# Kernel optimization log

Measured on AMD Instinct MI355X. Metric: run time of the kernel, lower is better.

Reference implementation:

```python
import jax, jax.numpy as jnp
import numpy as np

B, CIN, HIN, WIN = 1, 26, 721, 1440
K, HOUT, KH, KW = 9, 360, 9, 9
COUT = 256
PSCALE = WIN // (WIN // 2)  # lon downsample stride = 2
WOUT = WIN // 2


def setup_inputs() -> dict:
    key = jax.random.key(0)
    k1, k2, k3 = jax.random.split(key, 3)
    x = jax.random.normal(k1, (B, CIN, HIN, WIN), dtype=jnp.float32)
    # precomputed basis*quadrature stencil psi[k, ho, dh, dw] (shift-invariant in lon,
    # stored only for wo=0, exactly as DISCO does). Normalized per (k, ho) ('mean' mode).
    psi = jax.random.normal(k2, (K, HOUT, KH, KW), dtype=jnp.float32)
    psi = psi / (jnp.mean(jnp.abs(psi), axis=(2, 3), keepdims=True) * (KH * KW) + 1e-6)
    weight = jax.random.normal(k3, (COUT, CIN, K), dtype=jnp.float32) * (1.0 / np.sqrt(CIN * K))
    # base input-lat row for each output lat (stencil top row), clipped to valid range
    hi_base = np.clip(np.round(np.arange(HOUT) * (HIN - 1) / HOUT).astype(np.int32) - KH // 2, 0, HIN - 1)
    return {"x": x, "psi": psi, "weight": weight, "hi_base": jnp.asarray(hi_base, dtype=jnp.int32)}


def _disco_conv(x, psi, weight, hi_base):
    x = x.astype(jnp.float32)  # fp32 autocast-off region, matches torch module
    acc = jnp.zeros((B, CIN, K, HOUT, WOUT), dtype=jnp.float32)
    for dh in range(KH):  # small structural loop over stencil rows
        rows = jnp.clip(hi_base + dh, 0, HIN - 1)  # [Hout]
        xr = x[:, :, rows, :]
        for dw in range(KW):  # small structural loop over stencil lon offsets
            shift = dw - KW // 2
            xs = jnp.roll(xr, -shift, axis=-1)[..., ::PSCALE]  # [B,C,Hout,Wout]
            acc = acc + psi[:, :, dh, dw][None, None, :, :, None] * xs[:, :, None, :, :]
    # contract learned weights over kernel basis and input channels
    out = jnp.einsum('bckhw,ock->bohw', acc, weight)  # [B,Cout,Hout,Wout]
    return out


def reference(x, psi, weight, hi_base):
    return _disco_conv(x, psi, weight, hi_base)
```

## Files before the change

### kernel.cpp

```cpp
#include <hip/hip_runtime.h>
#include <hip/hip_bf16.h>

#define CIN_   26
#define HIN_   721
#define WIN_   1440
#define K_     9
#define HOUT_  360
#define KH_    9
#define KW_    9
#define COUT_  256
#define WOUT_  720

#define WT     16
#define XFP    40
#define CCH    7
#define CK     (CIN_ * K_)
#define NKS2   9
#define ACCP2  296
#define NMT    (COUT_ / 16)
#define NXCD   8
#define HBAND  (HOUT_ / NXCD)

typedef short bf16x8 __attribute__((ext_vector_type(8)));
typedef float f32x4  __attribute__((ext_vector_type(4)));

__device__ unsigned short g_whi[NMT * NKS2 * 64 * 8];
__device__ unsigned short g_pfrag[HOUT_ * 3 * 64 * 8];

__device__ __forceinline__ unsigned short f2bf_rne(float f) {
    union { float f; unsigned u; } v; v.f = f;
    unsigned u = v.u;
    unsigned r = (u + 0x7FFFu + ((u >> 16) & 1u)) >> 16;
    return (unsigned short)r;
}
__device__ __forceinline__ unsigned pack_bf2(float a, float b) {
    const __hip_bfloat162 bv = __float22bfloat162_rn(make_float2(a, b));
    return *reinterpret_cast<const unsigned*>(&bv);
}
__device__ __forceinline__ void gload_lds16(const float* g, float* l) {
    __builtin_amdgcn_global_load_lds(
        (const __attribute__((address_space(1))) void*)g,
        (__attribute__((address_space(3))) void*)l,
        16, 0, 0);
}

__global__ void prep_weight_kernel(const float* __restrict__ weight) {
    const int bid  = blockIdx.x;
    const int mt   = bid / NKS2;
    const int ks   = bid % NKS2;
    const int lane = threadIdx.x;
    const int row  = mt * 16 + (lane & 15);
    const int k0   = ks * 32 + (lane >> 4) * 8;
    const int base = ((mt * NKS2 + ks) * 64 + lane) * 8;
    #pragma unroll
    for (int j = 0; j < 8; ++j) {
        const int kp = k0 + j;
        float w = 0.f;
        if (kp < 260) {
            const int c = kp / 10, m = kp % 10;
            if (m < 9) w = weight[row * CK + c * 9 + m];
        }
        g_whi[base + j] = f2bf_rne(w);
    }
}

__global__ void prep_psi_kernel(const float* __restrict__ psi) {
    const int h    = blockIdx.x;
    const int lane = threadIdx.x;
    const int m    = lane & 15;
    const int kg   = lane >> 4;
    #pragma unroll
    for (int ks = 0; ks < 3; ++ks) {
        const int base = ((h * 3 + ks) * 64 + lane) * 8;
        #pragma unroll
        for (int e = 0; e < 8; ++e) {
            const int s = ks * 32 + kg * 8 + e;
            float v = 0.f;
            if (m < 9) {
                if (s < 72)      v = psi[(m * HOUT_ + h) * 81 + (s >> 3) * 9 + (s & 7)];
                else if (s < 81) v = psi[(m * HOUT_ + h) * 81 + (s - 72) * 9 + 8];
            }
            g_pfrag[base + e] = f2bf_rne(v);
        }
    }
}

#define LDS_BARRIER()                                      \
    do {                                                   \
        asm volatile("s_waitcnt lgkmcnt(0)" ::: "memory"); \
        __builtin_amdgcn_s_barrier();                      \
    } while (0)
#define VM_WAIT(N) asm volatile("s_waitcnt vmcnt(" #N ")" ::: "memory")

__global__ __launch_bounds__(256, 4)
void disco_fused_kernel(const float* __restrict__ x,
                        const int*   __restrict__ hi_base,
                        float* __restrict__ out)
{
    __shared__ float xs_f[2][12 * 256];
    __shared__ __align__(16) unsigned short acc_s[WT][ACCP2];

    const int b    = blockIdx.x;
    const int xcd  = b & (NXCD - 1);
    const int jb   = b >> 3;
    const int h    = xcd * HBAND + jb / 45;
    const int tile = jb % 45;
    const int w0   = tile * WT;
    const int tid  = threadIdx.x;

    const int hib = hi_base[h];

    #pragma unroll
    for (int t = 0; t < 2; ++t) {
        const int e = tid + t * 256;
        if (e < 16 * 28) acc_s[e / 28][260 + e % 28] = 0;
    }

    const int lane = tid & 63;
    const int wid  = tid >> 6;
    const int n    = lane & 15;
    const int kg   = lane >> 4;

    bf16x8 afrag[3];
    #pragma unroll
    for (int ks = 0; ks < 3; ++ks)
        afrag[ks] = *(const bf16x8*)&g_pfrag[((h * 3 + ks) * 64 + lane) * 8];
    VM_WAIT(0);

    const int c0 = 2 * w0 - 4;

    #define ISSUE_DMA(RD, BUF, RMAX)                                             \
    do {                                                                         \
        const int cb = (RD) * CCH;                                               \
        _Pragma("unroll")                                                        \
        for (int it = 0; it < 3; ++it) {                                         \
            const int g64 = wid + 4 * it;                                        \
            const int ii  = g64 * 64 + lane;                                     \
            int row = ii / 10;                                                   \
            const int q = ii - row * 10;                                         \
            if (row > (RMAX)) row = (RMAX);                                      \
            const int dh = row % 9;                                              \
            const int c  = cb + row / 9;                                         \
            int r = hib + dh;                                                    \
            if (r > HIN_ - 1) r = HIN_ - 1;                                      \
            int gc = c0 + 4 * q;                                                 \
            if (gc < 0)          gc += WIN_;                                     \
            else if (gc >= WIN_) gc -= WIN_;                                     \
            gload_lds16(x + ((size_t)c * HIN_ + r) * WIN_ + gc,                  \
                        &xs_f[BUF][g64 * 256]);                                  \
        }                                                                        \
    } while (0)

    ISSUE_DMA(0, 0, 62);
    ISSUE_DMA(1, 1, 62);
    VM_WAIT(3);
    LDS_BARRIER();

    #pragma unroll
    for (int rd = 0; rd < 4; ++rd) {
        const int nc = (rd == 3) ? (CIN_ - 3 * CCH) : CCH;
        const float* xsf = &xs_f[rd & 1][0];

        for (int cc = wid; cc < nc; cc += 4) {
            const int c = rd * CCH + cc;
            const float* rbase = xsf + (cc * 9) * XFP + 2 * n;
            f32x4 C = {0.f, 0.f, 0.f, 0.f};
            #pragma unroll
            for (int ks = 0; ks < 3; ++ks) {
                union { bf16x8 v; unsigned d[4]; unsigned short u[8]; } bf;
                if (ks < 2 || kg == 0) {
                    const float* rp = rbase + (ks * 4 + kg) * XFP;
                    #pragma unroll
                    for (int t = 0; t < 4; ++t) {
                        const float2 v2 = *reinterpret_cast<const float2*>(rp + 2 * t);
                        bf.d[t] = pack_bf2(v2.x, v2.y);
                    }
                } else if (kg == 1) {
                    #pragma unroll
                    for (int e = 0; e < 8; ++e)
                        bf.u[e] = f2bf_rne(rbase[e * XFP + 8]);
                } else if (kg == 2) {
                    bf.d[0] = bf.d[1] = bf.d[2] = bf.d[3] = 0;
                    bf.u[0] = f2bf_rne(rbase[8 * XFP + 8]);
                } else {
                    bf.d[0] = bf.d[1] = bf.d[2] = bf.d[3] = 0;
                }
                C = __builtin_amdgcn_mfma_f32_16x16x32_bf16(afrag[ks], bf.v, C, 0, 0, 0);
            }
            if (kg < 2) {
                unsigned* ap = reinterpret_cast<unsigned*>(&acc_s[n][c * 10 + kg * 4]);
                ap[0] = pack_bf2(C[0], C[1]);
                ap[1] = pack_bf2(C[2], C[3]);
            } else if (kg == 2) {
                *reinterpret_cast<unsigned*>(&acc_s[n][c * 10 + 8]) = pack_bf2(C[0], 0.f);
            }
        }

        if (rd == 0) {
            LDS_BARRIER();
            ISSUE_DMA(2, 0, 62);
            VM_WAIT(3);
            LDS_BARRIER();
        } else if (rd == 1) {
            LDS_BARRIER();
            ISSUE_DMA(3, 1, 44);
            VM_WAIT(3);
            LDS_BARRIER();
        } else if (rd == 2) {
            LDS_BARRIER();
            VM_WAIT(0);
            LDS_BARRIER();
        }
    }
    #undef ISSUE_DMA
    LDS_BARRIER();

    f32x4 C0 = {0.f, 0.f, 0.f, 0.f};
    f32x4 C1 = C0, C2 = C0, C3 = C0;

    const unsigned short* wp = g_whi + ((size_t)(wid * 4) * NKS2 * 64 + lane) * 8;

    bf16x8 wc[4];
    #pragma unroll
    for (int i = 0; i < 4; ++i)
        wc[i] = *(const bf16x8*)(wp + (size_t)i * NKS2 * 512);

    #pragma unroll
    for (int ks = 0; ks < NKS2; ++ks) {
        bf16x8 wn[4];
        if (ks + 1 < NKS2) {
            #pragma unroll
            for (int i = 0; i < 4; ++i)
                wn[i] = *(const bf16x8*)(wp + ((size_t)i * NKS2 + (ks + 1)) * 512);
        }
        const bf16x8 bhi = *(const bf16x8*)&acc_s[n][ks * 32 + kg * 8];
        C0 = __builtin_amdgcn_mfma_f32_16x16x32_bf16(wc[0], bhi, C0, 0, 0, 0);
        C1 = __builtin_amdgcn_mfma_f32_16x16x32_bf16(wc[1], bhi, C1, 0, 0, 0);
        C2 = __builtin_amdgcn_mfma_f32_16x16x32_bf16(wc[2], bhi, C2, 0, 0, 0);
        C3 = __builtin_amdgcn_mfma_f32_16x16x32_bf16(wc[3], bhi, C3, 0, 0, 0);
        if (ks + 1 < NKS2) {
            #pragma unroll
            for (int i = 0; i < 4; ++i) wc[i] = wn[i];
        }
    }

    #pragma unroll
    for (int i = 0; i < 4; ++i) {
        const f32x4 acc = (i == 0) ? C0 : (i == 1) ? C1 : (i == 2) ? C2 : C3;
        const int m0 = (wid * 4 + i) * 16 + kg * 4;
        #pragma unroll
        for (int r = 0; r < 4; ++r) {
            out[(size_t)(m0 + r) * (HOUT_ * WOUT_) + h * WOUT_ + w0 + n] = acc[r];
        }
    }
}

extern "C" void kernel_launch(void* const* d_in, const int* in_sizes, int n_in,
                              void* d_out, int out_size, void* d_ws, size_t ws_size,
                              hipStream_t stream)
{
    const float* x       = (const float*)d_in[0];
    const float* psi     = (const float*)d_in[1];
    const float* weight  = (const float*)d_in[2];
    const int*   hi_base = (const int*)d_in[3];
    float* out = (float*)d_out;

    hipLaunchKernelGGL(prep_weight_kernel, dim3(NMT * NKS2), dim3(64), 0, stream, weight);
    hipLaunchKernelGGL(prep_psi_kernel,    dim3(HOUT_),      dim3(64), 0, stream, psi);

    dim3 grid(45 * HOUT_, 1, 1);
    dim3 block(256, 1, 1);
    hipLaunchKernelGGL(disco_fused_kernel, grid, block, 0, stream,
                       x, hi_base, out);
}
```

Before: 257.1 us.

## Process five lon tiles per block with double-buffered accumulator and overlapped phases

Each block now loops over five consecutive longitude tiles for one output latitude, which shrinks the grid from 16200 to 3240 blocks and amortises the psi fragment, weight pointer and setup cost. The accumulator in LDS is double-buffered so the channel-mixing MFMA and output store for the previous tile run between the stencil rounds of the current tile. The input DMA for the next tile is also prefetched during the current tile. In exchange LDS use grows, occupancy is lowered to 3 blocks, and the per-block serial chain gets longer.

```diff
diff --git a/kernel.cpp b/kernel.cpp
--- a/kernel.cpp
+++ b/kernel.cpp
@@ -19,7 +19,7 @@
 #define ACCP2  296
 #define NMT    (COUT_ / 16)
 #define NXCD   8
-#define HBAND  (HOUT_ / NXCD)
+#define TPB    5
 
 typedef short bf16x8 __attribute__((ext_vector_type(8)));
 typedef float f32x4  __attribute__((ext_vector_type(4)));
@@ -92,167 +92,185 @@
     } while (0)
 #define VM_WAIT(N) asm volatile("s_waitcnt vmcnt(" #N ")" ::: "memory")
 
-__global__ __launch_bounds__(256, 4)
+#define ISSUE(C0V, RD, BUF, RMAX)                                                \
+do {                                                                             \
+    const int cb = (RD) * CCH;                                                   \
+    _Pragma("unroll")                                                            \
+    for (int it = 0; it < 3; ++it) {                                             \
+        const int g64 = wid + 4 * it;                                            \
+        const int ii  = g64 * 64 + lane;                                         \
+        int row = ii / 10;                                                       \
+        const int q = ii - row * 10;                                             \
+        if (row > (RMAX)) row = (RMAX);                                          \
+        const int dh = row % 9;                                                  \
+        const int c  = cb + row / 9;                                             \
+        int r = hib + dh;                                                        \
+        if (r > HIN_ - 1) r = HIN_ - 1;                                          \
+        int gc = (C0V) + 4 * q;                                                  \
+        if (gc < 0)          gc += WIN_;                                         \
+        else if (gc >= WIN_) gc -= WIN_;                                         \
+        gload_lds16(x + ((size_t)c * HIN_ + r) * WIN_ + gc,                      \
+                    &xs_f[BUF][g64 * 256]);                                      \
+    }                                                                            \
+} while (0)
+
+#define P1_ROUND(RD, BUF, ACC)                                                   \
+do {                                                                             \
+    const int nc = ((RD) == 3) ? (CIN_ - 3 * CCH) : CCH;                         \
+    const float* xsf = &xs_f[BUF][0];                                            \
+    for (int cc = wid; cc < nc; cc += 4) {                                       \
+        const int c = (RD) * CCH + cc;                                           \
+        const float* rbase = xsf + (cc * 9) * XFP + 2 * n;                       \
+        f32x4 C = {0.f, 0.f, 0.f, 0.f};                                          \
+        _Pragma("unroll")                                                        \
+        for (int ks = 0; ks < 3; ++ks) {                                         \
+            union { bf16x8 v; unsigned d[4]; unsigned short u[8]; } bf;          \
+            if (ks < 2 || kg == 0) {                                             \
+                const float* rp = rbase + (ks * 4 + kg) * XFP;                   \
+                _Pragma("unroll")                                                \
+                for (int t2 = 0; t2 < 4; ++t2) {                                 \
+                    const float2 v2 = *reinterpret_cast<const float2*>(rp + 2 * t2); \
+                    bf.d[t2] = pack_bf2(v2.x, v2.y);                             \
+                }                                                                \
+            } else if (kg == 1) {                                                \
+                _Pragma("unroll")                                                \
+                for (int e = 0; e < 8; ++e)                                      \
+                    bf.u[e] = f2bf_rne(rbase[e * XFP + 8]);                      \
+            } else if (kg == 2) {                                                \
+                bf.d[0] = bf.d[1] = bf.d[2] = bf.d[3] = 0;                       \
+                bf.u[0] = f2bf_rne(rbase[8 * XFP + 8]);                          \
+            } else {                                                             \
+                bf.d[0] = bf.d[1] = bf.d[2] = bf.d[3] = 0;                       \
+            }                                                                    \
+            C = __builtin_amdgcn_mfma_f32_16x16x32_bf16(afrag[ks], bf.v, C, 0, 0, 0); \
+        }                                                                        \
+        if (kg < 2) {                                                            \
+            unsigned* ap = reinterpret_cast<unsigned*>(&ACC[n][c * 10 + kg * 4]);\
+            ap[0] = pack_bf2(C[0], C[1]);                                        \
+            ap[1] = pack_bf2(C[2], C[3]);                                        \
+        } else if (kg == 2) {                                                    \
+            *reinterpret_cast<unsigned*>(&ACC[n][c * 10 + 8]) = pack_bf2(C[0], 0.f); \
+        }                                                                        \
+    }                                                                            \
+} while (0)
+
+#define P2_STORE(TT)                                                             \
+do {                                                                             \
+    const unsigned short (*accp)[ACCP2] =                                        \
+        (const unsigned short (*)[ACCP2])acc_s[(TT) & 1];                        \
+    f32x4 C0 = {0.f, 0.f, 0.f, 0.f}, C1 = C0, C2 = C0, C3 = C0;                  \
+    bf16x8 wc[4];                                                                \
+    _Pragma("unroll")                                                            \
+    for (int i = 0; i < 4; ++i)                                                  \
+        wc[i] = *(const bf16x8*)(wp + (size_t)i * NKS2 * 512);                   \
+    _Pragma("unroll")                                                            \
+    for (int ks = 0; ks < NKS2; ++ks) {                                          \
+        bf16x8 wn[4];                                                            \
+        if (ks + 1 < NKS2) {                                                     \
+            _Pragma("unroll")                                                    \
+            for (int i = 0; i < 4; ++i)                                          \
+                wn[i] = *(const bf16x8*)(wp + ((size_t)i * NKS2 + (ks + 1)) * 512); \
+        }                                                                        \
+        const bf16x8 bhi = *(const bf16x8*)&accp[n][ks * 32 + kg * 8];           \
+        C0 = __builtin_amdgcn_mfma_f32_16x16x32_bf16(wc[0], bhi, C0, 0, 0, 0);   \
+        C1 = __builtin_amdgcn_mfma_f32_16x16x32_bf16(wc[1], bhi, C1, 0, 0, 0);   \
+        C2 = __builtin_amdgcn_mfma_f32_16x16x32_bf16(wc[2], bhi, C2, 0, 0, 0);   \
+        C3 = __builtin_amdgcn_mfma_f32_16x16x32_bf16(wc[3], bhi, C3, 0, 0, 0);   \
+        if (ks + 1 < NKS2) {                                                     \
+            _Pragma("unroll")                                                    \
+            for (int i = 0; i < 4; ++i) wc[i] = wn[i];                           \
+        }                                                                        \
+    }                                                                            \
+    const int w0s = (tile0 + (TT)) * WT;                                         \
+    _Pragma("unroll")                                                            \
+    for (int i = 0; i < 4; ++i) {                                                \
+        const f32x4 a2 = (i == 0) ? C0 : (i == 1) ? C1 : (i == 2) ? C2 : C3;     \
+        const int m0 = (wid * 4 + i) * 16 + kg * 4;                              \
+        _Pragma("unroll")                                                        \
+        for (int r = 0; r < 4; ++r)                                              \
+            out[(size_t)(m0 + r) * (HOUT_ * WOUT_) + h * WOUT_ + w0s + n] = a2[r]; \
+    }                                                                            \
+} while (0)
+
+__global__ __launch_bounds__(256, 3)
 void disco_fused_kernel(const float* __restrict__ x,
                         const int*   __restrict__ hi_base,
                         float* __restrict__ out)
 {
     __shared__ float xs_f[2][12 * 256];
-    __shared__ __align__(16) unsigned short acc_s[WT][ACCP2];
-
-    const int b    = blockIdx.x;
-    const int xcd  = b & (NXCD - 1);
-    const int jb   = b >> 3;
-    const int h    = xcd * HBAND + jb / 45;
-    const int tile = jb % 45;
-    const int w0   = tile * WT;
-    const int tid  = threadIdx.x;
+    __shared__ __align__(16) unsigned short acc_s[2][WT][ACCP2];
+
+    const int b     = blockIdx.x;
+    const int xcd   = b & (NXCD - 1);
+    const int j     = b >> 3;
+    const int h     = xcd * 45 + j / 9;
+    const int tile0 = (j % 9) * TPB;
+    const int tid   = threadIdx.x;
 
     const int hib = hi_base[h];
-
-    #pragma unroll
-    for (int t = 0; t < 2; ++t) {
-        const int e = tid + t * 256;
-        if (e < 16 * 28) acc_s[e / 28][260 + e % 28] = 0;
-    }
 
     const int lane = tid & 63;
     const int wid  = tid >> 6;
     const int n    = lane & 15;
     const int kg   = lane >> 4;
 
+    for (int e = tid; e < 2 * 16 * 28; e += 256)
+        acc_s[e / 448][(e % 448) / 28][260 + (e % 28)] = 0;
+
     bf16x8 afrag[3];
     #pragma unroll
     for (int ks = 0; ks < 3; ++ks)
         afrag[ks] = *(const bf16x8*)&g_pfrag[((h * 3 + ks) * 64 + lane) * 8];
+    const unsigned short* wp = g_whi + ((size_t)(wid * 4) * NKS2 * 64 + lane) * 8;
     VM_WAIT(0);
 
-    const int c0 = 2 * w0 - 4;
-
-    #define ISSUE_DMA(RD, BUF, RMAX)                                             \
-    do {                                                                         \
-        const int cb = (RD) * CCH;                                               \
-        _Pragma("unroll")                                                        \
-        for (int it = 0; it < 3; ++it) {                                         \
-            const int g64 = wid + 4 * it;                                        \
-            const int ii  = g64 * 64 + lane;                                     \
-            int row = ii / 10;                                                   \
-            const int q = ii - row * 10;                                         \
-            if (row > (RMAX)) row = (RMAX);                                      \
-            const int dh = row % 9;                                              \
-            const int c  = cb + row / 9;                                         \
-            int r = hib + dh;                                                    \
-            if (r > HIN_ - 1) r = HIN_ - 1;                                      \
-            int gc = c0 + 4 * q;                                                 \
-            if (gc < 0)          gc += WIN_;                                     \
-            else if (gc >= WIN_) gc -= WIN_;                                     \
-            gload_lds16(x + ((size_t)c * HIN_ + r) * WIN_ + gc,                  \
-                        &xs_f[BUF][g64 * 256]);                                  \
-        }                                                                        \
-    } while (0)
-
-    ISSUE_DMA(0, 0, 62);
-    ISSUE_DMA(1, 1, 62);
-    VM_WAIT(3);
-    LDS_BARRIER();
-
-    #pragma unroll
-    for (int rd = 0; rd < 4; ++rd) {
-        const int nc = (rd == 3) ? (CIN_ - 3 * CCH) : CCH;
-        const float* xsf = &xs_f[rd & 1][0];
-
-        for (int cc = wid; cc < nc; cc += 4) {
-            const int c = rd * CCH + cc;
-            const float* rbase = xsf + (cc * 9) * XFP + 2 * n;
-            f32x4 C = {0.f, 0.f, 0.f, 0.f};
-            #pragma unroll
-            for (int ks = 0; ks < 3; ++ks) {
-                union { bf16x8 v; unsigned d[4]; unsigned short u[8]; } bf;
-                if (ks < 2 || kg == 0) {
-                    const float* rp = rbase + (ks * 4 + kg) * XFP;
-                    #pragma unroll
-                    for (int t = 0; t < 4; ++t) {
-                        const float2 v2 = *reinterpret_cast<const float2*>(rp + 2 * t);
-                        bf.d[t] = pack_bf2(v2.x, v2.y);
-                    }
-                } else if (kg == 1) {
-                    #pragma unroll
-                    for (int e = 0; e < 8; ++e)
-                        bf.u[e] = f2bf_rne(rbase[e * XFP + 8]);
-                } else if (kg == 2) {
-                    bf.d[0] = bf.d[1] = bf.d[2] = bf.d[3] = 0;
-                    bf.u[0] = f2bf_rne(rbase[8 * XFP + 8]);
-                } else {
-                    bf.d[0] = bf.d[1] = bf.d[2] = bf.d[3] = 0;
-                }
-                C = __builtin_amdgcn_mfma_f32_16x16x32_bf16(afrag[ks], bf.v, C, 0, 0, 0);
-            }
-            if (kg < 2) {
-                unsigned* ap = reinterpret_cast<unsigned*>(&acc_s[n][c * 10 + kg * 4]);
-                ap[0] = pack_bf2(C[0], C[1]);
-                ap[1] = pack_bf2(C[2], C[3]);
-            } else if (kg == 2) {
-                *reinterpret_cast<unsigned*>(&acc_s[n][c * 10 + 8]) = pack_bf2(C[0], 0.f);
-            }
-        }
-
-        if (rd == 0) {
-            LDS_BARRIER();
-            ISSUE_DMA(2, 0, 62);
+    for (int t = 0; t < TPB; ++t) {
+        const int c0  = 2 * (tile0 + t) * WT - 4;
+        const int c0n = 2 * (tile0 + t + 1) * WT - 4;
+        unsigned short (*acc)[ACCP2] = acc_s[t & 1];
+
+        if (t == 0) {
+            ISSUE(c0, 0, 0, 62);
+            ISSUE(c0, 1, 1, 62);
             VM_WAIT(3);
             LDS_BARRIER();
-        } else if (rd == 1) {
-            LDS_BARRIER();
-            ISSUE_DMA(3, 1, 44);
+        }
+
+        P1_ROUND(0, 0, acc);
+        LDS_BARRIER();
+        ISSUE(c0, 2, 0, 62);
+        VM_WAIT(3);
+        LDS_BARRIER();
+
+        P1_ROUND(1, 1, acc);
+        LDS_BARRIER();
+        ISSUE(c0, 3, 1, 44);
+        VM_WAIT(3);
+        LDS_BARRIER();
+
+        P1_ROUND(2, 0, acc);
+        LDS_BARRIER();
+        if (t + 1 < TPB) {
+            ISSUE(c0n, 0, 0, 62);
             VM_WAIT(3);
-            LDS_BARRIER();
-        } else if (rd == 2) {
-            LDS_BARRIER();
+        } else {
             VM_WAIT(0);
-            LDS_BARRIER();
-        }
+        }
+        LDS_BARRIER();
+
+        if (t > 0) P2_STORE(t - 1);
+
+        P1_ROUND(3, 1, acc);
+        LDS_BARRIER();
+        if (t + 1 < TPB) {
+            ISSUE(c0n, 1, 1, 62);
+            VM_WAIT(3);
+        } else {
+            VM_WAIT(0);
+        }
+        LDS_BARRIER();
     }
-    #undef ISSUE_DMA
-    LDS_BARRIER();
-
-    f32x4 C0 = {0.f, 0.f, 0.f, 0.f};
-    f32x4 C1 = C0, C2 = C0, C3 = C0;
-
-    const unsigned short* wp = g_whi + ((size_t)(wid * 4) * NKS2 * 64 + lane) * 8;
-
-    bf16x8 wc[4];
-    #pragma unroll
-    for (int i = 0; i < 4; ++i)
-        wc[i] = *(const bf16x8*)(wp + (size_t)i * NKS2 * 512);
-
-    #pragma unroll
-    for (int ks = 0; ks < NKS2; ++ks) {
-        bf16x8 wn[4];
-        if (ks + 1 < NKS2) {
-            #pragma unroll
-            for (int i = 0; i < 4; ++i)
-                wn[i] = *(const bf16x8*)(wp + ((size_t)i * NKS2 + (ks + 1)) * 512);
-        }
-        const bf16x8 bhi = *(const bf16x8*)&acc_s[n][ks * 32 + kg * 8];
-        C0 = __builtin_amdgcn_mfma_f32_16x16x32_bf16(wc[0], bhi, C0, 0, 0, 0);
-        C1 = __builtin_amdgcn_mfma_f32_16x16x32_bf16(wc[1], bhi, C1, 0, 0, 0);
-        C2 = __builtin_amdgcn_mfma_f32_16x16x32_bf16(wc[2], bhi, C2, 0, 0, 0);
-        C3 = __builtin_amdgcn_mfma_f32_16x16x32_bf16(wc[3], bhi, C3, 0, 0, 0);
-        if (ks + 1 < NKS2) {
-            #pragma unroll
-            for (int i = 0; i < 4; ++i) wc[i] = wn[i];
-        }
-    }
-
-    #pragma unroll
-    for (int i = 0; i < 4; ++i) {
-        const f32x4 acc = (i == 0) ? C0 : (i == 1) ? C1 : (i == 2) ? C2 : C3;
-        const int m0 = (wid * 4 + i) * 16 + kg * 4;
-        #pragma unroll
-        for (int r = 0; r < 4; ++r) {
-            out[(size_t)(m0 + r) * (HOUT_ * WOUT_) + h * WOUT_ + w0 + n] = acc[r];
-        }
-    }
+    P2_STORE(TPB - 1);
 }
 
 extern "C" void kernel_launch(void* const* d_in, const int* in_sizes, int n_in,
@@ -268,8 +286,6 @@
     hipLaunchKernelGGL(prep_weight_kernel, dim3(NMT * NKS2), dim3(64), 0, stream, weight);
     hipLaunchKernelGGL(prep_psi_kernel,    dim3(HOUT_),      dim3(64), 0, stream, psi);
 
-    dim3 grid(45 * HOUT_, 1, 1);
-    dim3 block(256, 1, 1);
-    hipLaunchKernelGGL(disco_fused_kernel, grid, block, 0, stream,
+    hipLaunchKernelGGL(disco_fused_kernel, dim3(3240), dim3(256), 0, stream,
                        x, hi_base, out);
 }
```

Measured after the change: 380.3 us. 48.0% more time.
